# Kernel optimization log

Measured on AMD Instinct MI355X. Metric: run time of the kernel, lower is better.

Reference implementation:

```python
import jax, jax.numpy as jnp
import numpy as np

N_NODES = 100000
N_EDGES = 3200000


def _gcn_layer(x, W, b, src, dst, n):
    # DGL GraphConv, norm='both': D_out^{-1/2} A^T D_in^{-1/2} style normalization.
    ones = jnp.ones((src.shape[0],), dtype=x.dtype)
    deg_out = jnp.clip(jax.ops.segment_sum(ones, src, num_segments=n), 1.0)  # out-degree of src
    deg_in = jnp.clip(jax.ops.segment_sum(ones, dst, num_segments=n), 1.0)   # in-degree of dst
    # pre-normalize and project first (in_feats >= out_feats => cheaper messages)
    h = (x * jax.lax.rsqrt(deg_out)[:, None]) @ W            # [N, out]
    agg = jax.ops.segment_sum(h[src], dst, num_segments=n)   # gather + scatter-add over edges
    return agg * jax.lax.rsqrt(deg_in)[:, None] + b


def setup_inputs() -> dict:
    key = jax.random.key(0)
    k1, k2, k3, k4, k5 = jax.random.split(key, 5)
    in_f, h_f, n_cls = 256, 128, 40
    x = jax.random.normal(k1, (N_NODES, in_f), dtype=jnp.float32)
    W1 = jax.random.normal(k2, (in_f, h_f), dtype=jnp.float32) * (1.0 / np.sqrt(in_f))
    b1 = jnp.zeros((h_f,), dtype=jnp.float32)
    W2 = jax.random.normal(k3, (h_f, n_cls), dtype=jnp.float32) * (1.0 / np.sqrt(h_f))
    b2 = jnp.zeros((n_cls,), dtype=jnp.float32)
    src = jax.random.randint(k4, (N_EDGES,), 0, N_NODES, dtype=jnp.int32)
    dst = jax.random.randint(k5, (N_EDGES,), 0, N_NODES, dtype=jnp.int32)
    return {"x": x, "W1": W1, "b1": b1, "W2": W2, "b2": b2, "src": src, "dst": dst}


def reference(x, W1, b1, W2, b2, src, dst):
    n = x.shape[0]
    h = _gcn_layer(x, W1, b1, src, dst, n)
    h = jax.nn.relu(h)
    return _gcn_layer(h, W2, b2, src, dst, n)  # [N, num_classes] logits
```

## Files before the change

kernel.cpp:

```cpp
#include <hip/hip_runtime.h>

#define IN_F 256
#define HID  128
#define NCLS 40
#define NBKT 256
#define BKTSH 9
#define CH 8192
#define CAP 18432

typedef __attribute__((ext_vector_type(8))) short bf16x8;
typedef __attribute__((ext_vector_type(4))) float f32x4;

static __device__ __forceinline__ unsigned short f2bf(float f) {
    unsigned u = __builtin_bit_cast(unsigned, f);
    u += 0x7fffu + ((u >> 16) & 1u);
    return (unsigned short)(u >> 16);
}
static __device__ __forceinline__ float bf2f(unsigned short b) {
    return __builtin_bit_cast(float, ((unsigned)b) << 16);
}

__global__ void initcur_kernel(int* __restrict__ curD, int* __restrict__ curS) {
    int t = threadIdx.x;
    curD[t] = t * CAP;
    curS[t] = t * CAP;
}

__global__ __launch_bounds__(256) void binBoth_kernel(
    const int* __restrict__ src, const int* __restrict__ dst,
    int* __restrict__ curD, int* __restrict__ curS,
    int* __restrict__ bin, unsigned short* __restrict__ bin2, int E) {
    __shared__ int sS[CH];
    __shared__ int sD[CH];
    __shared__ int cntD[NBKT], ofsD[NBKT];
    __shared__ int cntS[NBKT], ofsS[NBKT];
    const int tx = threadIdx.x;
    const int be = blockIdx.x * CH;
    const int n  = min(CH, E - be);
    cntD[tx] = 0; cntS[tx] = 0;
    __syncthreads();
    for (int i = tx; i < n; i += 256) {
        int d = dst[be + i], s = src[be + i];
        sD[i] = d; sS[i] = s;
        atomicAdd(&cntD[d >> BKTSH], 1);
        atomicAdd(&cntS[s >> BKTSH], 1);
    }
    __syncthreads();
    int c = cntD[tx];
    ofsD[tx] = c ? atomicAdd(&curD[tx], c) : 0;
    cntD[tx] = 0;
    c = cntS[tx];
    ofsS[tx] = c ? atomicAdd(&curS[tx], c) : 0;
    cntS[tx] = 0;
    __syncthreads();
    for (int i = tx; i < n; i += 256) {
        int d = sD[i], s = sS[i];
        int b = d >> BKTSH;
        int l = atomicAdd(&cntD[b], 1);
        bin[ofsD[b] + l] = ((d & 511) << 17) | s;
        int b2 = s >> BKTSH;
        int l2 = atomicAdd(&cntS[b2], 1);
        bin2[ofsS[b2] + l2] = (unsigned short)(s & 511);
    }
}

__global__ __launch_bounds__(256) void passB_kernel(
    const int* __restrict__ curD_final, const int* __restrict__ bin,
    int* __restrict__ csr_src, int* __restrict__ row_ptr, int* __restrict__ row_end,
    float* __restrict__ rs_in, int N) {
    __shared__ int cnt[512];
    __shared__ int cur[512];
    __shared__ int part[256];
    const int b = blockIdx.x;
    const int base = b * CAP, end = curD_final[b];
    const int tx = threadIdx.x;
    cnt[tx] = 0; cnt[tx + 256] = 0;
    __syncthreads();
    for (int i = base + tx; i < end; i += 256)
        atomicAdd(&cnt[bin[i] >> 17], 1);
    __syncthreads();
    int a0 = cnt[2 * tx], a1 = cnt[2 * tx + 1];
    part[tx] = a0 + a1;
    __syncthreads();
    for (int off = 1; off < 256; off <<= 1) {
        int v = (tx >= off) ? part[tx - off] : 0;
        __syncthreads();
        part[tx] += v;
        __syncthreads();
    }
    int excl = part[tx] - (a0 + a1);
    cur[2 * tx] = excl;
    cur[2 * tx + 1] = excl + a0;
    int idx = (b << BKTSH) + 2 * tx;
    row_ptr[idx]     = base + excl;
    row_end[idx]     = base + excl + a0;
    row_ptr[idx + 1] = base + excl + a0;
    row_end[idx + 1] = base + excl + a0 + a1;
    if (idx < N)     rs_in[idx]     = rsqrtf((float)max(a0, 1));
    if (idx + 1 < N) rs_in[idx + 1] = rsqrtf((float)max(a1, 1));
    __syncthreads();
    for (int i = base + tx; i < end; i += 256) {
        int v = bin[i];
        int nl = v >> 17;
        int p = atomicAdd(&cur[nl], 1);
        csr_src[base + p] = v & 0x1FFFF;
    }
}

__global__ __launch_bounds__(256) void passBs_kernel(
    const int* __restrict__ curS_final, const unsigned short* __restrict__ bin2,
    float* __restrict__ rs_out, int N) {
    __shared__ int cnt[512];
    const int b = blockIdx.x;
    const int base = b * CAP, end = curS_final[b];
    const int tx = threadIdx.x;
    cnt[tx] = 0; cnt[tx + 256] = 0;
    __syncthreads();
    for (int i = base + tx; i < end; i += 256)
        atomicAdd(&cnt[bin2[i]], 1);
    __syncthreads();
    int idx = (b << BKTSH) + tx;
    if (idx < N)       rs_out[idx]       = rsqrtf((float)max(cnt[tx], 1));
    if (idx + 256 < N) rs_out[idx + 256] = rsqrtf((float)max(cnt[tx + 256], 1));
}

__global__ __launch_bounds__(256) void gemm1_kernel(
    const float* __restrict__ x, const float* __restrict__ W1,
    const float* __restrict__ rs_out, unsigned short* __restrict__ h1b, int N) {
    __shared__ unsigned short Wl[32768];

    const int tx = threadIdx.x;
#pragma unroll
    for (int e = 0; e < 32; ++e) {
        int base = (tx + 256 * e) * 4;
        float4 w = *(const float4*)&W1[base];
        int k = base >> 7;
        int c0 = base & 127;
        float wv[4] = {w.x, w.y, w.z, w.w};
#pragma unroll
        for (int q = 0; q < 4; ++q) {
            int col = c0 + q;
            int byte = col * 512 + k * 2;
            byte ^= (col & 7) << 4;
            Wl[byte >> 1] = f2bf(wv[q]);
        }
    }
    __syncthreads();

    const int wv_ = tx >> 6, lane = tx & 63;

    for (int t = 0; t < 2; ++t) {
        const int r0 = blockIdx.x * 128 + t * 64 + wv_ * 16;
        const int arow = r0 + (lane & 15);
        const int arow_c = min(arow, N - 1);
        const float rs = rs_out[arow_c];
        const long xbase = (long)arow_c * IN_F + (lane >> 4) * 8;

        bf16x8 a8[8];
#pragma unroll
        for (int ks = 0; ks < 8; ++ks) {
            float4 p0 = *(const float4*)&x[xbase + ks * 32];
            float4 p1 = *(const float4*)&x[xbase + ks * 32 + 4];
            bf16x8 a;
            a[0] = (short)f2bf(p0.x * rs); a[1] = (short)f2bf(p0.y * rs);
            a[2] = (short)f2bf(p0.z * rs); a[3] = (short)f2bf(p0.w * rs);
            a[4] = (short)f2bf(p1.x * rs); a[5] = (short)f2bf(p1.y * rs);
            a[6] = (short)f2bf(p1.z * rs); a[7] = (short)f2bf(p1.w * rs);
            a8[ks] = a;
        }

        f32x4 acc[8];
#pragma unroll
        for (int nf = 0; nf < 8; ++nf) acc[nf] = (f32x4){0.f, 0.f, 0.f, 0.f};

#pragma unroll
        for (int ks = 0; ks < 8; ++ks) {
#pragma unroll
            for (int nf = 0; nf < 8; ++nf) {
                int col = nf * 16 + (lane & 15);
                int kb  = ks * 32 + (lane >> 4) * 8;
                int byte = col * 512 + kb * 2;
                byte ^= (col & 7) << 4;
                bf16x8 b = *(const bf16x8*)((const char*)Wl + byte);
                acc[nf] = __builtin_amdgcn_mfma_f32_16x16x32_bf16(a8[ks], b, acc[nf], 0, 0, 0);
            }
        }

#pragma unroll
        for (int nf = 0; nf < 8; ++nf) {
#pragma unroll
            for (int j = 0; j < 4; ++j) {
                int row = r0 + (lane >> 4) * 4 + j;
                if (row < N)
                    h1b[(long)row * HID + nf * 16 + (lane & 15)] = f2bf(acc[nf][j]);
            }
        }
    }
}

__global__ __launch_bounds__(256) void agg1_kernel(
    const int* __restrict__ row_ptr, const int* __restrict__ row_end,
    const int* __restrict__ csr_src, const unsigned* __restrict__ h1b2,
    unsigned* __restrict__ aggb, int N) {
    int node = (blockIdx.x * 256 + threadIdx.x) >> 6;
    int lane = threadIdx.x & 63;
    if (node >= N) return;
    int e = row_ptr[node], end = row_end[node];
    float ax = 0.f, ay = 0.f;
    for (; e + 8 <= end; e += 8) {
        int s0 = csr_src[e],     s1 = csr_src[e + 1], s2 = csr_src[e + 2], s3 = csr_src[e + 3];
        int s4 = csr_src[e + 4], s5 = csr_src[e + 5], s6 = csr_src[e + 6], s7 = csr_src[e + 7];
        unsigned u0 = h1b2[(long)s0 * 64 + lane];
        unsigned u1 = h1b2[(long)s1 * 64 + lane];
        unsigned u2 = h1b2[(long)s2 * 64 + lane];
        unsigned u3 = h1b2[(long)s3 * 64 + lane];
        unsigned u4 = h1b2[(long)s4 * 64 + lane];
        unsigned u5 = h1b2[(long)s5 * 64 + lane];
        unsigned u6 = h1b2[(long)s6 * 64 + lane];
        unsigned u7 = h1b2[(long)s7 * 64 + lane];
        ax += (__builtin_bit_cast(float, u0 << 16) + __builtin_bit_cast(float, u1 << 16))
            + (__builtin_bit_cast(float, u2 << 16) + __builtin_bit_cast(float, u3 << 16))
            + (__builtin_bit_cast(float, u4 << 16) + __builtin_bit_cast(float, u5 << 16))
            + (__builtin_bit_cast(float, u6 << 16) + __builtin_bit_cast(float, u7 << 16));
        ay += (__builtin_bit_cast(float, u0 & 0xffff0000u) + __builtin_bit_cast(float, u1 & 0xffff0000u))
            + (__builtin_bit_cast(float, u2 & 0xffff0000u) + __builtin_bit_cast(float, u3 & 0xffff0000u))
            + (__builtin_bit_cast(float, u4 & 0xffff0000u) + __builtin_bit_cast(float, u5 & 0xffff0000u))
            + (__builtin_bit_cast(float, u6 & 0xffff0000u) + __builtin_bit_cast(float, u7 & 0xffff0000u));
    }
    for (; e < end; ++e) {
        unsigned u = h1b2[(long)csr_src[e] * 64 + lane];
        ax += __builtin_bit_cast(float, u << 16);
        ay += __builtin_bit_cast(float, u & 0xffff0000u);
    }
    aggb[(long)node * 64 + lane] = ((unsigned)f2bf(ay) << 16) | (unsigned)f2bf(ax);
}

__global__ __launch_bounds__(256) void gemm2_kernel(
    const unsigned short* __restrict__ aggb, const float* __restrict__ W2,
    const float* __restrict__ b1, const float* __restrict__ rs_in,
    const float* __restrict__ rs_out, unsigned short* __restrict__ h2p, int N) {
    __shared__ unsigned short Wl[48 * 128];

    const int tx = threadIdx.x;
    for (int idx = tx; idx < 48 * 128; idx += 256) Wl[idx] = 0;
    __syncthreads();
    for (int idx = tx; idx < 128 * NCLS; idx += 256) {
        int k = idx / NCLS, c = idx - k * NCLS;
        int byte = c * 256 + k * 2;
        byte ^= (c & 7) << 4;
        Wl[byte >> 1] = f2bf(W2[idx]);
    }
    __syncthreads();

    const int wv_ = tx >> 6, lane = tx & 63;
    const int r0 = blockIdx.x * 64 + wv_ * 16;
    const int arow = r0 + (lane & 15);
    const int arow_c = min(arow, N - 1);
    const float ri = rs_in[arow_c];
    const float ro = rs_out[arow_c];
    const int k0 = (lane >> 4) * 8;
    const long abase = (long)arow_c * HID + k0;

    bf16x8 a8[4];
#pragma unroll
    for (int ks = 0; ks < 4; ++ks) {
        bf16x8 ar = *(const bf16x8*)&aggb[abase + ks * 32];
        float4 c0 = *(const float4*)&b1[k0 + ks * 32];
        float4 c1 = *(const float4*)&b1[k0 + ks * 32 + 4];
        float bv[8] = {c0.x, c0.y, c0.z, c0.w, c1.x, c1.y, c1.z, c1.w};
        bf16x8 a;
#pragma unroll
        for (int j = 0; j < 8; ++j)
            a[j] = (short)f2bf(fmaxf(fmaf(bf2f((unsigned short)ar[j]), ri, bv[j]), 0.f) * ro);
        a8[ks] = a;
    }

    f32x4 acc[3];
#pragma unroll
    for (int nf = 0; nf < 3; ++nf) acc[nf] = (f32x4){0.f, 0.f, 0.f, 0.f};

#pragma unroll
    for (int ks = 0; ks < 4; ++ks) {
#pragma unroll
        for (int nf = 0; nf < 3; ++nf) {
            int col = nf * 16 + (lane & 15);
            int kb  = ks * 32 + k0;
            int byte = col * 256 + kb * 2;
            byte ^= (col & 7) << 4;
            bf16x8 b = *(const bf16x8*)((const char*)Wl + byte);
            acc[nf] = __builtin_amdgcn_mfma_f32_16x16x32_bf16(a8[ks], b, acc[nf], 0, 0, 0);
        }
    }

#pragma unroll
    for (int nf = 0; nf < 3; ++nf) {
        int col = nf * 16 + (lane & 15);
        if (col < NCLS) {
#pragma unroll
            for (int j = 0; j < 4; ++j) {
                int row = r0 + (lane >> 4) * 4 + j;
                if (row < N)
                    h2p[(long)row * 64 + col] = f2bf(acc[nf][j]);
            }
        }
    }
}

__global__ __launch_bounds__(256) void agg2_kernel(
    const int* __restrict__ row_ptr, const int* __restrict__ row_end,
    const int* __restrict__ csr_src, const unsigned* __restrict__ h2p2,
    const float* __restrict__ rs_in, const float* __restrict__ b2,
    float* __restrict__ out, int N) {
    int i = blockIdx.x * 256 + threadIdx.x;
    if (i >= N * 20) return;
    int node = i / 20;
    int cp   = i - node * 20;
    int e = row_ptr[node], end = row_end[node];
    float ax = 0.f, ay = 0.f;
    for (; e + 8 <= end; e += 8) {
        int s0 = csr_src[e],     s1 = csr_src[e + 1], s2 = csr_src[e + 2], s3 = csr_src[e + 3];
        int s4 = csr_src[e + 4], s5 = csr_src[e + 5], s6 = csr_src[e + 6], s7 = csr_src[e + 7];
        unsigned u0 = h2p2[(long)s0 * 32 + cp];
        unsigned u1 = h2p2[(long)s1 * 32 + cp];
        unsigned u2 = h2p2[(long)s2 * 32 + cp];
        unsigned u3 = h2p2[(long)s3 * 32 + cp];
        unsigned u4 = h2p2[(long)s4 * 32 + cp];
        unsigned u5 = h2p2[(long)s5 * 32 + cp];
        unsigned u6 = h2p2[(long)s6 * 32 + cp];
        unsigned u7 = h2p2[(long)s7 * 32 + cp];
        ax += (__builtin_bit_cast(float, u0 << 16) + __builtin_bit_cast(float, u1 << 16))
            + (__builtin_bit_cast(float, u2 << 16) + __builtin_bit_cast(float, u3 << 16))
            + (__builtin_bit_cast(float, u4 << 16) + __builtin_bit_cast(float, u5 << 16))
            + (__builtin_bit_cast(float, u6 << 16) + __builtin_bit_cast(float, u7 << 16));
        ay += (__builtin_bit_cast(float, u0 & 0xffff0000u) + __builtin_bit_cast(float, u1 & 0xffff0000u))
            + (__builtin_bit_cast(float, u2 & 0xffff0000u) + __builtin_bit_cast(float, u3 & 0xffff0000u))
            + (__builtin_bit_cast(float, u4 & 0xffff0000u) + __builtin_bit_cast(float, u5 & 0xffff0000u))
            + (__builtin_bit_cast(float, u6 & 0xffff0000u) + __builtin_bit_cast(float, u7 & 0xffff0000u));
    }
    for (; e < end; ++e) {
        unsigned u = h2p2[(long)csr_src[e] * 32 + cp];
        ax += __builtin_bit_cast(float, u << 16);
        ay += __builtin_bit_cast(float, u & 0xffff0000u);
    }
    float r = rs_in[node];
    float2 o;
    o.x = fmaf(ax, r, b2[2 * cp]);
    o.y = fmaf(ay, r, b2[2 * cp + 1]);
    *(float2*)&out[(long)node * NCLS + 2 * cp] = o;
}

extern "C" void kernel_launch(void* const* d_in, const int* in_sizes, int n_in,
                              void* d_out, int out_size, void* d_ws, size_t ws_size,
                              hipStream_t stream) {
    const float* x  = (const float*)d_in[0];
    const float* W1 = (const float*)d_in[1];
    const float* b1 = (const float*)d_in[2];
    const float* W2 = (const float*)d_in[3];
    const float* b2 = (const float*)d_in[4];
    const int*  src = (const int*)d_in[5];
    const int*  dst = (const int*)d_in[6];
    const int N = in_sizes[0] / IN_F;
    const int E = in_sizes[5];
    const int NBLK = (N + 511) >> BKTSH;

    float* wsf       = (float*)d_ws;
    float* rs_out    = wsf;
    float* rs_in     = wsf + N;
    int*   curD      = (int*)(wsf + 2 * (long)N);
    int*   curS      = curD + NBKT;
    int*   row_ptr   = curS + NBKT;
    int*   row_end   = row_ptr + N + 1024;
    int*   bin       = row_end + N + 1024;
    int*   csr_src   = bin + (long)NBLK * CAP;
    unsigned short* bin2 = (unsigned short*)(csr_src + (long)NBLK * CAP);
    unsigned short* h1b  = bin2 + (long)NBLK * CAP;
    unsigned short* aggb = h1b + (long)N * HID;
    unsigned short* h2p  = aggb + (long)N * HID;

    initcur_kernel<<<1, 256, 0, stream>>>(curD, curS);
    binBoth_kernel<<<(E + CH - 1) / CH, 256, 0, stream>>>(src, dst, curD, curS,
                                                          bin, bin2, E);
    passB_kernel<<<NBLK, 256, 0, stream>>>(curD, bin, csr_src, row_ptr, row_end, rs_in, N);
    passBs_kernel<<<NBLK, 256, 0, stream>>>(curS, bin2, rs_out, N);

    gemm1_kernel<<<(N + 127) / 128, 256, 0, stream>>>(x, W1, rs_out, h1b, N);
    agg1_kernel<<<(N * 64 + 255) / 256, 256, 0, stream>>>(row_ptr, row_end, csr_src,
                                                          (const unsigned*)h1b,
                                                          (unsigned*)aggb, N);
    gemm2_kernel<<<(N + 63) / 64, 256, 0, stream>>>(aggb, W2, b1, rs_in, rs_out, h2p, N);
    agg2_kernel<<<(N * 20 + 255) / 256, 256, 0, stream>>>(row_ptr, row_end, csr_src,
                                                          (const unsigned*)h2p, rs_in, b2,
                                                          (float*)d_out, N);
}
```

Before: 356.9 us.

## Fuse degree passes, enlarge gemm1 row tile, use packed bf16 conversion

Merges the destination CSR-build pass and the source-degree pass into a single kernel, removing one launch. gemm1 now processes 256 rows per block instead of 128, which halves the number of times the W1 tile is staged into LDS. Float-to-bf16 rounding now goes through the packed __float22bfloat162_rn intrinsic instead of manual bit arithmetic. The fused pass runs its two phases serially within each block, and the larger gemm1 tile cuts the block count, which may reduce occupancy.

```diff
diff --git a/kernel.cpp b/kernel.cpp
--- a/kernel.cpp
+++ b/kernel.cpp
@@ -1,4 +1,5 @@
 #include <hip/hip_runtime.h>
+#include <hip/hip_bf16.h>
 
 #define IN_F 256
 #define HID  128
@@ -18,6 +19,13 @@
 }
 static __device__ __forceinline__ float bf2f(unsigned short b) {
     return __builtin_bit_cast(float, ((unsigned)b) << 16);
+}
+static __device__ __forceinline__ unsigned pk2(float lo, float hi) {
+    float2 t; t.x = lo; t.y = hi;
+    __hip_bfloat162 h = __float22bfloat162_rn(t);
+    unsigned r;
+    __builtin_memcpy(&r, &h, 4);
+    return r;
 }
 
 __global__ void initcur_kernel(int* __restrict__ curD, int* __restrict__ curS) {
@@ -64,16 +72,18 @@
     }
 }
 
-__global__ __launch_bounds__(256) void passB_kernel(
-    const int* __restrict__ curD_final, const int* __restrict__ bin,
+__global__ __launch_bounds__(256) void passBoth_kernel(
+    const int* __restrict__ curD_final, const int* __restrict__ curS_final,
+    const int* __restrict__ bin, const unsigned short* __restrict__ bin2,
     int* __restrict__ csr_src, int* __restrict__ row_ptr, int* __restrict__ row_end,
-    float* __restrict__ rs_in, int N) {
+    float* __restrict__ rs_in, float* __restrict__ rs_out, int N) {
     __shared__ int cnt[512];
     __shared__ int cur[512];
     __shared__ int part[256];
     const int b = blockIdx.x;
-    const int base = b * CAP, end = curD_final[b];
     const int tx = threadIdx.x;
+    const int base = b * CAP;
+    const int end = curD_final[b];
     cnt[tx] = 0; cnt[tx + 256] = 0;
     __syncthreads();
     for (int i = base + tx; i < end; i += 256)
@@ -101,27 +111,19 @@
     __syncthreads();
     for (int i = base + tx; i < end; i += 256) {
         int v = bin[i];
-        int nl = v >> 17;
-        int p = atomicAdd(&cur[nl], 1);
+        int p = atomicAdd(&cur[v >> 17], 1);
         csr_src[base + p] = v & 0x1FFFF;
     }
-}
-
-__global__ __launch_bounds__(256) void passBs_kernel(
-    const int* __restrict__ curS_final, const unsigned short* __restrict__ bin2,
-    float* __restrict__ rs_out, int N) {
-    __shared__ int cnt[512];
-    const int b = blockIdx.x;
-    const int base = b * CAP, end = curS_final[b];
-    const int tx = threadIdx.x;
+    __syncthreads();
     cnt[tx] = 0; cnt[tx + 256] = 0;
     __syncthreads();
-    for (int i = base + tx; i < end; i += 256)
+    const int endS = curS_final[b];
+    for (int i = base + tx; i < endS; i += 256)
         atomicAdd(&cnt[bin2[i]], 1);
     __syncthreads();
-    int idx = (b << BKTSH) + tx;
-    if (idx < N)       rs_out[idx]       = rsqrtf((float)max(cnt[tx], 1));
-    if (idx + 256 < N) rs_out[idx + 256] = rsqrtf((float)max(cnt[tx + 256], 1));
+    int idx2 = (b << BKTSH) + tx;
+    if (idx2 < N)       rs_out[idx2]       = rsqrtf((float)max(cnt[tx], 1));
+    if (idx2 + 256 < N) rs_out[idx2 + 256] = rsqrtf((float)max(cnt[tx + 256], 1));
 }
 
 __global__ __launch_bounds__(256) void gemm1_kernel(
@@ -149,8 +151,8 @@
 
     const int wv_ = tx >> 6, lane = tx & 63;
 
-    for (int t = 0; t < 2; ++t) {
-        const int r0 = blockIdx.x * 128 + t * 64 + wv_ * 16;
+    for (int t = 0; t < 4; ++t) {
+        const int r0 = blockIdx.x * 256 + t * 64 + wv_ * 16;
         const int arow = r0 + (lane & 15);
         const int arow_c = min(arow, N - 1);
         const float rs = rs_out[arow_c];
@@ -161,12 +163,12 @@
         for (int ks = 0; ks < 8; ++ks) {
             float4 p0 = *(const float4*)&x[xbase + ks * 32];
             float4 p1 = *(const float4*)&x[xbase + ks * 32 + 4];
-            bf16x8 a;
-            a[0] = (short)f2bf(p0.x * rs); a[1] = (short)f2bf(p0.y * rs);
-            a[2] = (short)f2bf(p0.z * rs); a[3] = (short)f2bf(p0.w * rs);
-            a[4] = (short)f2bf(p1.x * rs); a[5] = (short)f2bf(p1.y * rs);
-            a[6] = (short)f2bf(p1.z * rs); a[7] = (short)f2bf(p1.w * rs);
-            a8[ks] = a;
+            union { unsigned u[4]; bf16x8 v; } au;
+            au.u[0] = pk2(p0.x * rs, p0.y * rs);
+            au.u[1] = pk2(p0.z * rs, p0.w * rs);
+            au.u[2] = pk2(p1.x * rs, p1.y * rs);
+            au.u[3] = pk2(p1.z * rs, p1.w * rs);
+            a8[ks] = au.v;
         }
 
         f32x4 acc[8];
@@ -232,7 +234,7 @@
         ax += __builtin_bit_cast(float, u << 16);
         ay += __builtin_bit_cast(float, u & 0xffff0000u);
     }
-    aggb[(long)node * 64 + lane] = ((unsigned)f2bf(ay) << 16) | (unsigned)f2bf(ax);
+    aggb[(long)node * 64 + lane] = pk2(ax, ay);
 }
 
 __global__ __launch_bounds__(256) void gemm2_kernel(
@@ -268,11 +270,16 @@
         float4 c0 = *(const float4*)&b1[k0 + ks * 32];
         float4 c1 = *(const float4*)&b1[k0 + ks * 32 + 4];
         float bv[8] = {c0.x, c0.y, c0.z, c0.w, c1.x, c1.y, c1.z, c1.w};
-        bf16x8 a;
+        float f[8];
 #pragma unroll
         for (int j = 0; j < 8; ++j)
-            a[j] = (short)f2bf(fmaxf(fmaf(bf2f((unsigned short)ar[j]), ri, bv[j]), 0.f) * ro);
-        a8[ks] = a;
+            f[j] = fmaxf(fmaf(bf2f((unsigned short)ar[j]), ri, bv[j]), 0.f) * ro;
+        union { unsigned u[4]; bf16x8 v; } au;
+        au.u[0] = pk2(f[0], f[1]);
+        au.u[1] = pk2(f[2], f[3]);
+        au.u[2] = pk2(f[4], f[5]);
+        au.u[3] = pk2(f[6], f[7]);
+        a8[ks] = au.v;
     }
 
     f32x4 acc[3];
@@ -380,10 +387,10 @@
     initcur_kernel<<<1, 256, 0, stream>>>(curD, curS);
     binBoth_kernel<<<(E + CH - 1) / CH, 256, 0, stream>>>(src, dst, curD, curS,
                                                           bin, bin2, E);
-    passB_kernel<<<NBLK, 256, 0, stream>>>(curD, bin, csr_src, row_ptr, row_end, rs_in, N);
-    passBs_kernel<<<NBLK, 256, 0, stream>>>(curS, bin2, rs_out, N);
-
-    gemm1_kernel<<<(N + 127) / 128, 256, 0, stream>>>(x, W1, rs_out, h1b, N);
+    passBoth_kernel<<<NBLK, 256, 0, stream>>>(curD, curS, bin, bin2, csr_src,
+                                              row_ptr, row_end, rs_in, rs_out, N);
+
+    gemm1_kernel<<<(N + 255) / 256, 256, 0, stream>>>(x, W1, rs_out, h1b, N);
     agg1_kernel<<<(N * 64 + 255) / 256, 256, 0, stream>>>(row_ptr, row_end, csr_src,
                                                           (const unsigned*)h1b,
                                                           (unsigned*)aggb, N);
```

After: 345.5 us. 1.03x faster.
